# Optimization experiments

Measured on AMD Instinct MI355X. Metric: run time of the kernel, lower is better.

Reference implementation:

```python
import jax, jax.numpy as jnp
import numpy as np

N_HEADS = 2

def setup_inputs() -> dict:
    key = jax.random.key(0)
    ks = jax.random.split(key, 10)
    d, bank, b, t = 192, 1000, 16, 4096
    s = 1.0 / np.sqrt(d)
    return {
        "z": jax.random.normal(ks[0], (b, d, t), jnp.float32),
        "memory_bank": jax.random.normal(ks[1], (d, bank), jnp.float32),
        "Wq": jax.random.normal(ks[2], (d, d), jnp.float32) * s,
        "bq": jax.random.normal(ks[3], (d,), jnp.float32) * 0.02,
        "Wk": jax.random.normal(ks[4], (d, d), jnp.float32) * s,
        "bk": jax.random.normal(ks[5], (d,), jnp.float32) * 0.02,
        "Wv": jax.random.normal(ks[6], (d, d), jnp.float32) * s,
        "bv": jax.random.normal(ks[7], (d,), jnp.float32) * 0.02,
        "Wo": jax.random.normal(ks[8], (d, d), jnp.float32) * s,
        "bo": jax.random.normal(ks[9], (d,), jnp.float32) * 0.02,
    }


def _split_heads(x):
    # x: [b, d, t] -> [b, h, t, dk]  (matches view(b, h, dk, t).transpose(2, 3))
    b, d, t = x.shape
    dk = d // N_HEADS
    return x.reshape(b, N_HEADS, dk, t).transpose(0, 1, 3, 2)


def reference(z, memory_bank, Wq, bq, Wk, bk, Wv, bv, Wo, bo):
    b, d, t = z.shape
    dk = d // N_HEADS
    # memory bank expanded over batch: [b, d, bank]
    c = jnp.broadcast_to(memory_bank[None], (b,) + memory_bank.shape)
    # 1x1 conv projections == per-channel linear
    q = jnp.einsum('oc,bct->bot', Wq, z) + bq[None, :, None]
    k = jnp.einsum('oc,bcs->bos', Wk, c) + bk[None, :, None]
    v = jnp.einsum('oc,bcs->bos', Wv, c) + bv[None, :, None]
    qh = _split_heads(q)  # [b, h, t, dk]
    kh = _split_heads(k)  # [b, h, bank, dk]
    vh = _split_heads(v)  # [b, h, bank, dk]
    scores = jnp.einsum('bhtd,bhsd->bhts', qh, kh) / jnp.sqrt(jnp.asarray(dk, z.dtype))
    p = jax.nn.softmax(scores, axis=-1)  # [b, h, t, bank]
    out = jnp.einsum('bhts,bhsd->bhtd', p, vh)  # [b, h, t, dk]
    out = out.transpose(0, 1, 3, 2).reshape(b, d, t)  # merge heads -> [b, d, t]
    return jnp.einsum('oc,bct->bot', Wo, out) + bo[None, :, None]
```

## Files before the change

### kernel.cpp

```cpp
#include <hip/hip_runtime.h>


typedef float  f32x4  __attribute__((ext_vector_type(4)));
typedef __bf16 bf16;
typedef __bf16 bf16x8 __attribute__((ext_vector_type(8)));

#define B_   16
#define D_   192
#define T_   4096
#define BANK 1000
#define SP   1024
#define DK   96
#define SCALE 0.10206207261596577f
#define LOG2E 1.4426950408889634f

__global__ __launch_bounds__(256) void kv_kernel(
    const float* __restrict__ mb, const float* __restrict__ Wk, const float* __restrict__ bk,
    const float* __restrict__ Wv, const float* __restrict__ bv,
    bf16* __restrict__ ktg, bf16* __restrict__ vtg) {
  int s = blockIdx.x * 256 + threadIdx.x;
  int o = blockIdx.y;
  int h = o / DK, i = o % DK;
  float ak = 0.f, av = 0.f;
  if (s < BANK) {
    ak = bk[o]; av = bv[o];
    for (int c = 0; c < D_; ++c) {
      float m = mb[c * BANK + s];
      ak += Wk[o * D_ + c] * m;
      av += Wv[o * D_ + c] * m;
    }
  }
  ktg[(size_t)(h * SP + s) * DK + i] = (bf16)ak;
  vtg[(size_t)(h * DK + i) * SP + s] = (bf16)av;
}

__global__ __launch_bounds__(256) void zt_kernel(const float* __restrict__ z,
                                                 bf16* __restrict__ zT) {
  __shared__ __align__(16) bf16 sT[64 * 200];
  const int tid = threadIdx.x;
  const int t0 = blockIdx.x * 64, b = blockIdx.y;
#pragma unroll
  for (int it = 0; it < 48; ++it) {
    int e = tid + 256 * it;
    int c = e >> 6, tl = e & 63;
    sT[tl * 200 + c] = (bf16)z[((size_t)b * D_ + c) * T_ + t0 + tl];
  }
  __syncthreads();
#pragma unroll
  for (int it = 0; it < 6; ++it) {
    int g = tid + 256 * it;
    int tl = g / 24, c8 = (g % 24) * 8;
    bf16x8 v = *(const bf16x8*)&sT[tl * 200 + c8];
    *(bf16x8*)&zT[((size_t)b * T_ + t0 + tl) * D_ + c8] = v;
  }
}

template <typename OT>
__global__ __launch_bounds__(256) void proj_kernel(
    const bf16* __restrict__ XT, const float* __restrict__ W,
    const float* __restrict__ bias, OT* __restrict__ Y, float outscale) {
  __shared__ __align__(16) char smem[40960];
  bf16* sA = (bf16*)smem;
  bf16* sB = (bf16*)(smem + 16384);
  float* sE = (float*)smem;

  const int tid = threadIdx.x;
  const int t0 = blockIdx.x * 256, o0 = blockIdx.y * 64, b = blockIdx.z;
  const int lane = tid & 63, wv = tid >> 6;
  const int quad = lane >> 4, l15 = lane & 15;

#pragma unroll
  for (int r = 0; r < 6; ++r) {
    int g = tid + 256 * r;
    int kb = g >> 8, nt = (g >> 6) & 3, qd = (g >> 4) & 3, l5 = g & 15;
    const float* wp = &W[(o0 + nt * 16 + l5) * D_ + kb * 32 + qd * 8];
    f32x4 wa = *(const f32x4*)wp, wb = *(const f32x4*)(wp + 4);
    bf16x8 pk;
#pragma unroll
    for (int u = 0; u < 4; ++u) { pk[u] = (bf16)wa[u]; pk[4 + u] = (bf16)wb[u]; }
    *(bf16x8*)&sB[(size_t)g * 8] = pk;
  }

  f32x4 acc[4][4];
#pragma unroll
  for (int m = 0; m < 4; ++m)
#pragma unroll
    for (int n = 0; n < 4; ++n) acc[m][n] = (f32x4){0.f, 0.f, 0.f, 0.f};

  for (int kb = 0; kb < 6; ++kb) {
    __syncthreads();
#pragma unroll
    for (int r = 0; r < 4; ++r) {
      int g = tid + 256 * r;
      int tg = g >> 6, qd = (g >> 4) & 3, l5 = g & 15;
      bf16x8 v = *(const bf16x8*)&XT[((size_t)b * T_ + t0 + tg * 16 + l5) * D_ +
                                     kb * 32 + qd * 8];
      *(bf16x8*)&sA[(size_t)g * 8] = v;
    }
    __syncthreads();
    bf16x8 bf[4];
#pragma unroll
    for (int n = 0; n < 4; ++n)
      bf[n] = *(const bf16x8*)&sB[(size_t)((kb * 4 + n) * 64 + lane) * 8];
#pragma unroll
    for (int m = 0; m < 4; ++m) {
      bf16x8 af = *(const bf16x8*)&sA[(size_t)((wv * 4 + m) * 64 + lane) * 8];
#pragma unroll
      for (int n = 0; n < 4; ++n)
        acc[m][n] = __builtin_amdgcn_mfma_f32_16x16x32_bf16(af, bf[n], acc[m][n], 0, 0, 0);
    }
  }
  __syncthreads();

  float bs[4];
#pragma unroll
  for (int n = 0; n < 4; ++n) bs[n] = bias[o0 + n * 16 + l15];
  float* se = sE + wv * 1088;
#pragma unroll
  for (int m = 0; m < 4; ++m) {
#pragma unroll
    for (int n = 0; n < 4; ++n)
#pragma unroll
      for (int r = 0; r < 4; ++r)
        se[(quad * 4 + r) * 68 + n * 16 + l15] = (acc[m][n][r] + bs[n]) * outscale;
#pragma unroll
    for (int oo = 0; oo < 16; ++oo) {
      int ol = oo * 4 + quad;
      Y[((size_t)b * D_ + o0 + ol) * T_ + t0 + wv * 64 + m * 16 + l15] =
          (OT)se[l15 * 68 + ol];
    }
  }
}

__global__ __launch_bounds__(512) void attn_kernel(
    const bf16* __restrict__ qws, const bf16* __restrict__ ktg,
    const bf16* __restrict__ vtg, bf16* __restrict__ owsT) {
  __shared__ __align__(16) char smem[32768];
  bf16* kt = (bf16*)smem;
  bf16* vt = (bf16*)(smem + 12288);
  bf16* sP = (bf16*)(smem + 24576);
  bf16* qt = (bf16*)smem;

  const int tid = threadIdx.x;
  const int t0 = blockIdx.x * 128, h = blockIdx.y, b = blockIdx.z;
  const int lane = tid & 63, wv = tid >> 6;
  const int quad = lane >> 4, l15 = lane & 15;

  const bf16* kb_g = ktg + (size_t)h * SP * DK;
  const bf16* vb_g = vtg + (size_t)h * DK * SP;

  const bf16* sp_ptr[3];
  int sp_str[3];
#pragma unroll
  for (int r = 0; r < 3; ++r) {
    int g = tid + 512 * r;
    if (g < 768) {
      int kb = g >> 8, n = (g >> 6) & 3, qd = (g >> 4) & 3, l5 = g & 15;
      sp_ptr[r] = kb_g + (size_t)(n * 16 + l5) * DK + kb * 32 + qd * 8;
      sp_str[r] = 64 * DK;
    } else {
      int gv = g - 768, blk = gv >> 6;
      int kbv = blk / 6, n = blk % 6, qd = (gv >> 4) & 3, l5 = gv & 15;
      sp_ptr[r] = vb_g + (size_t)(n * 16 + l5) * SP + kbv * 32 + qd * 8;
      sp_str[r] = 64;
    }
  }
  bf16x8 kreg[3];
#pragma unroll
  for (int r = 0; r < 3; ++r) kreg[r] = *(const bf16x8*)sp_ptr[r];

#pragma unroll
  for (int r = 0; r < 3; ++r) {
    int g8 = tid + 512 * r;
    int i = g8 >> 4, t8 = (g8 & 15) * 8;
    bf16x8 v = *(const bf16x8*)&qws[((size_t)(b * D_ + h * DK + i)) * T_ + t0 + t8];
    int kb = i >> 5, qd = (i >> 3) & 3, j = i & 7;
#pragma unroll
    for (int tt = 0; tt < 8; ++tt) {
      int t = t8 + tt;
      qt[(size_t)((kb * 8 + (t >> 4)) * 64 + qd * 16 + (t & 15)) * 8 + j] = v[tt];
    }
  }
  __syncthreads();
  bf16x8 qf[3];
#pragma unroll
  for (int kb = 0; kb < 3; ++kb)
    qf[kb] = *(const bf16x8*)&qt[(size_t)((kb * 8 + wv) * 64 + lane) * 8];

  f32x4 oacc[6];
#pragma unroll
  for (int n = 0; n < 6; ++n) oacc[n] = (f32x4){0.f, 0.f, 0.f, 0.f};
  float m_run[4] = {-1e30f, -1e30f, -1e30f, -1e30f};
  float l_run[4] = {0.f, 0.f, 0.f, 0.f};

  for (int ch = 0; ch < 16; ++ch) {
    __syncthreads();
#pragma unroll
    for (int r = 0; r < 3; ++r)
      *(bf16x8*)(smem + (size_t)(tid + 512 * r) * 16) = kreg[r];
    __syncthreads();
    if (ch < 15) {
#pragma unroll
      for (int r = 0; r < 3; ++r) {
        sp_ptr[r] += sp_str[r];
        kreg[r] = *(const bf16x8*)sp_ptr[r];
      }
    }

    f32x4 sacc[4];
#pragma unroll
    for (int n = 0; n < 4; ++n) sacc[n] = (f32x4){0.f, 0.f, 0.f, 0.f};
#pragma unroll
    for (int kb = 0; kb < 3; ++kb) {
#pragma unroll
      for (int n = 0; n < 4; ++n) {
        bf16x8 bfm = *(const bf16x8*)&kt[(size_t)((kb * 4 + n) * 64 + lane) * 8];
        sacc[n] = __builtin_amdgcn_mfma_f32_16x16x32_bf16(qf[kb], bfm, sacc[n], 0, 0, 0);
      }
    }
    if (ch == 15) {
#pragma unroll
      for (int r = 0; r < 4; ++r) {
        if (l15 >= 8) sacc[2][r] = -1e30f;
        sacc[3][r] = -1e30f;
      }
    }

    float mc[4];
#pragma unroll
    for (int r = 0; r < 4; ++r) {
      float m0 = fmaxf(fmaxf(sacc[0][r], sacc[1][r]), fmaxf(sacc[2][r], sacc[3][r]));
      m0 = fmaxf(m0, __shfl_xor(m0, 1, 64));
      m0 = fmaxf(m0, __shfl_xor(m0, 2, 64));
      m0 = fmaxf(m0, __shfl_xor(m0, 4, 64));
      m0 = fmaxf(m0, __shfl_xor(m0, 8, 64));
      mc[r] = m0;
    }
    bool keep = (mc[0] - m_run[0] <= 8.f) && (mc[1] - m_run[1] <= 8.f) &&
                (mc[2] - m_run[2] <= 8.f) && (mc[3] - m_run[3] <= 8.f);
    if (!__all(keep)) {
#pragma unroll
      for (int r = 0; r < 4; ++r) {
        float mn = fmaxf(m_run[r], mc[r]);
        float al = exp2f(m_run[r] - mn);
        m_run[r] = mn;
        l_run[r] *= al;
#pragma unroll
        for (int n = 0; n < 6; ++n) oacc[n][r] *= al;
      }
    }
    float pr[4][4];
#pragma unroll
    for (int r = 0; r < 4; ++r) {
      float ls = 0.f;
#pragma unroll
      for (int n = 0; n < 4; ++n) { pr[n][r] = exp2f(sacc[n][r] - m_run[r]); ls += pr[n][r]; }
      ls += __shfl_xor(ls, 1, 64);
      ls += __shfl_xor(ls, 2, 64);
      ls += __shfl_xor(ls, 4, 64);
      ls += __shfl_xor(ls, 8, 64);
      l_run[r] += ls;
    }

#pragma unroll
    for (int kb = 0; kb < 2; ++kb) {
#pragma unroll
      for (int nn = 0; nn < 2; ++nn) {
        int n = kb * 2 + nn;
        int qd2 = (nn << 1) | (l15 >> 3), j = l15 & 7;
#pragma unroll
        for (int r = 0; r < 4; ++r)
          sP[(size_t)(wv * 64 + qd2 * 16 + quad * 4 + (r ^ quad)) * 8 + j] =
              (bf16)pr[n][r];
      }
      bf16x8 pa = *(const bf16x8*)&sP[(size_t)(wv * 64 + (lane ^ ((lane >> 2) & 3))) * 8];
#pragma unroll
      for (int n2 = 0; n2 < 6; ++n2) {
        bf16x8 vf = *(const bf16x8*)&vt[(size_t)((kb * 6 + n2) * 64 + lane) * 8];
        oacc[n2] = __builtin_amdgcn_mfma_f32_16x16x32_bf16(pa, vf, oacc[n2], 0, 0, 0);
      }
    }
  }

  float inv[4];
#pragma unroll
  for (int r = 0; r < 4; ++r) inv[r] = 1.0f / l_run[r];
  __syncthreads();
  bf16* sOw = (bf16*)smem + wv * (96 * 17);
#pragma unroll
  for (int n2 = 0; n2 < 6; ++n2)
#pragma unroll
    for (int r = 0; r < 4; ++r)
      sOw[(n2 * 16 + l15) * 17 + quad * 4 + r] = (bf16)(oacc[n2][r] * inv[r]);
#pragma unroll
  for (int r2 = 0; r2 < 24; ++r2) {
    int g = r2 * 64 + lane;
    int tl = g / 96, i = g % 96;
    owsT[((size_t)b * T_ + t0 + wv * 16 + tl) * D_ + h * DK + i] = sOw[i * 17 + tl];
  }
}

extern "C" void kernel_launch(void* const* d_in, const int* in_sizes, int n_in,
                              void* d_out, int out_size, void* d_ws, size_t ws_size,
                              hipStream_t stream) {
  const float* z  = (const float*)d_in[0];
  const float* mb = (const float*)d_in[1];
  const float* Wq = (const float*)d_in[2];
  const float* bq = (const float*)d_in[3];
  const float* Wk = (const float*)d_in[4];
  const float* bk = (const float*)d_in[5];
  const float* Wv = (const float*)d_in[6];
  const float* bv = (const float*)d_in[7];
  const float* Wo = (const float*)d_in[8];
  const float* bo = (const float*)d_in[9];
  float* out = (float*)d_out;

  bf16* ktg  = (bf16*)d_ws;
  bf16* vtg  = ktg + 2 * SP * DK;
  bf16* zT   = vtg + 2 * DK * SP;
  bf16* owsT = zT + (size_t)B_ * T_ * D_;
  bf16* qws  = owsT + (size_t)B_ * T_ * D_;

  kv_kernel        <<<dim3(SP / 256, D_),    256, 0, stream>>>(mb, Wk, bk, Wv, bv, ktg, vtg);
  zt_kernel        <<<dim3(T_ / 64, B_),     256, 0, stream>>>(z, zT);
  proj_kernel<bf16><<<dim3(T_ / 256, 3, B_), 256, 0, stream>>>(zT, Wq, bq, qws, SCALE * LOG2E);
  attn_kernel      <<<dim3(T_ / 128, 2, B_), 512, 0, stream>>>(qws, ktg, vtg, owsT);
  proj_kernel<float><<<dim3(T_ / 256, 3, B_), 256, 0, stream>>>(owsT, Wo, bo, out, 1.0f);
}
```

Measured before the change: 300.0 us.

## Merge KV and transpose launches, prefetch proj operands, swizzle attention LDS

Merges the K/V projection kernel and the z transpose kernel into a single launch, with blocks picking their role from blockIdx.y. This removes one kernel launch and lets the two independent jobs run at the same time. The projection GEMM now loads the next k-block of activations into registers before the MFMAs run, overlapping global loads with compute. The attention kernel's Q and P shared-memory layouts gain XOR swizzles meant to cut LDS bank conflicts, at the cost of extra index arithmetic and register pressure.

```diff
diff --git a/kernel.cpp b/kernel.cpp
--- a/kernel.cpp
+++ b/kernel.cpp
@@ -14,44 +14,46 @@
 #define SCALE 0.10206207261596577f
 #define LOG2E 1.4426950408889634f
 
-__global__ __launch_bounds__(256) void kv_kernel(
-    const float* __restrict__ mb, const float* __restrict__ Wk, const float* __restrict__ bk,
+__global__ __launch_bounds__(256) void pre_kernel(
+    const float* __restrict__ z, bf16* __restrict__ zT,
+    const float* __restrict__ mb,
+    const float* __restrict__ Wk, const float* __restrict__ bk,
     const float* __restrict__ Wv, const float* __restrict__ bv,
     bf16* __restrict__ ktg, bf16* __restrict__ vtg) {
-  int s = blockIdx.x * 256 + threadIdx.x;
-  int o = blockIdx.y;
-  int h = o / DK, i = o % DK;
-  float ak = 0.f, av = 0.f;
-  if (s < BANK) {
-    ak = bk[o]; av = bv[o];
-    for (int c = 0; c < D_; ++c) {
-      float m = mb[c * BANK + s];
-      ak += Wk[o * D_ + c] * m;
-      av += Wv[o * D_ + c] * m;
-    }
-  }
-  ktg[(size_t)(h * SP + s) * DK + i] = (bf16)ak;
-  vtg[(size_t)(h * DK + i) * SP + s] = (bf16)av;
-}
-
-__global__ __launch_bounds__(256) void zt_kernel(const float* __restrict__ z,
-                                                 bf16* __restrict__ zT) {
   __shared__ __align__(16) bf16 sT[64 * 200];
   const int tid = threadIdx.x;
-  const int t0 = blockIdx.x * 64, b = blockIdx.y;
-#pragma unroll
-  for (int it = 0; it < 48; ++it) {
-    int e = tid + 256 * it;
-    int c = e >> 6, tl = e & 63;
-    sT[tl * 200 + c] = (bf16)z[((size_t)b * D_ + c) * T_ + t0 + tl];
-  }
-  __syncthreads();
-#pragma unroll
-  for (int it = 0; it < 6; ++it) {
-    int g = tid + 256 * it;
-    int tl = g / 24, c8 = (g % 24) * 8;
-    bf16x8 v = *(const bf16x8*)&sT[tl * 200 + c8];
-    *(bf16x8*)&zT[((size_t)b * T_ + t0 + tl) * D_ + c8] = v;
+  if (blockIdx.y < 16) {
+    const int t0 = blockIdx.x * 64, b = blockIdx.y;
+#pragma unroll
+    for (int it = 0; it < 48; ++it) {
+      int e = tid + 256 * it;
+      int c = e >> 6, tl = e & 63;
+      sT[tl * 200 + c] = (bf16)z[((size_t)b * D_ + c) * T_ + t0 + tl];
+    }
+    __syncthreads();
+#pragma unroll
+    for (int it = 0; it < 6; ++it) {
+      int g = tid + 256 * it;
+      int tl = g / 24, c8 = (g % 24) * 8;
+      bf16x8 v = *(const bf16x8*)&sT[tl * 200 + c8];
+      *(bf16x8*)&zT[((size_t)b * T_ + t0 + tl) * D_ + c8] = v;
+    }
+  } else {
+    int idx = (blockIdx.y - 16) * 64 + blockIdx.x;
+    int s = (idx & 3) * 256 + tid;
+    int o = idx >> 2;
+    int h = o / DK, i = o % DK;
+    float ak = 0.f, av = 0.f;
+    if (s < BANK) {
+      ak = bk[o]; av = bv[o];
+      for (int c = 0; c < D_; ++c) {
+        float m = mb[c * BANK + s];
+        ak += Wk[o * D_ + c] * m;
+        av += Wv[o * D_ + c] * m;
+      }
+    }
+    ktg[(size_t)(h * SP + s) * DK + i] = (bf16)ak;
+    vtg[(size_t)(h * DK + i) * SP + s] = (bf16)av;
   }
 }
 
@@ -69,6 +71,17 @@
   const int lane = tid & 63, wv = tid >> 6;
   const int quad = lane >> 4, l15 = lane & 15;
 
+  const bf16* ap[4];
+#pragma unroll
+  for (int r = 0; r < 4; ++r) {
+    int g = tid + 256 * r;
+    int tg = g >> 6, qd = (g >> 4) & 3, l5 = g & 15;
+    ap[r] = &XT[((size_t)b * T_ + t0 + tg * 16 + l5) * D_ + qd * 8];
+  }
+  bf16x8 areg[4];
+#pragma unroll
+  for (int r = 0; r < 4; ++r) areg[r] = *(const bf16x8*)ap[r];
+
 #pragma unroll
   for (int r = 0; r < 6; ++r) {
     int g = tid + 256 * r;
@@ -90,14 +103,14 @@
   for (int kb = 0; kb < 6; ++kb) {
     __syncthreads();
 #pragma unroll
-    for (int r = 0; r < 4; ++r) {
-      int g = tid + 256 * r;
-      int tg = g >> 6, qd = (g >> 4) & 3, l5 = g & 15;
-      bf16x8 v = *(const bf16x8*)&XT[((size_t)b * T_ + t0 + tg * 16 + l5) * D_ +
-                                     kb * 32 + qd * 8];
-      *(bf16x8*)&sA[(size_t)g * 8] = v;
-    }
-    __syncthreads();
+    for (int r = 0; r < 4; ++r)
+      *(bf16x8*)&sA[(size_t)(tid + 256 * r) * 8] = areg[r];
+    __syncthreads();
+    if (kb < 5) {
+#pragma unroll
+      for (int r = 0; r < 4; ++r)
+        areg[r] = *(const bf16x8*)(ap[r] + (kb + 1) * 32);
+    }
     bf16x8 bf[4];
 #pragma unroll
     for (int n = 0; n < 4; ++n)
@@ -178,14 +191,19 @@
 #pragma unroll
     for (int tt = 0; tt < 8; ++tt) {
       int t = t8 + tt;
-      qt[(size_t)((kb * 8 + (t >> 4)) * 64 + qd * 16 + (t & 15)) * 8 + j] = v[tt];
+      int G = (kb * 8 + (t >> 4)) * 64 + qd * 16 + (t & 15);
+      int Gs = G ^ ((G >> 6) & 7);
+      qt[(size_t)Gs * 8 + j] = v[tt];
     }
   }
   __syncthreads();
   bf16x8 qf[3];
 #pragma unroll
-  for (int kb = 0; kb < 3; ++kb)
-    qf[kb] = *(const bf16x8*)&qt[(size_t)((kb * 8 + wv) * 64 + lane) * 8];
+  for (int kb = 0; kb < 3; ++kb) {
+    int G = (kb * 8 + wv) * 64 + lane;
+    int Gs = G ^ ((G >> 6) & 7);
+    qf[kb] = *(const bf16x8*)&qt[(size_t)Gs * 8];
+  }
 
   f32x4 oacc[6];
 #pragma unroll
@@ -269,11 +287,14 @@
         int n = kb * 2 + nn;
         int qd2 = (nn << 1) | (l15 >> 3), j = l15 & 7;
 #pragma unroll
-        for (int r = 0; r < 4; ++r)
-          sP[(size_t)(wv * 64 + qd2 * 16 + quad * 4 + (r ^ quad)) * 8 + j] =
-              (bf16)pr[n][r];
-      }
-      bf16x8 pa = *(const bf16x8*)&sP[(size_t)(wv * 64 + (lane ^ ((lane >> 2) & 3))) * 8];
+        for (int r = 0; r < 4; ++r) {
+          int g0 = qd2 * 16 + quad * 4 + r;
+          int gs = g0 ^ ((g0 >> 3) & 7);
+          sP[(size_t)(wv * 64 + gs) * 8 + j] = (bf16)pr[n][r];
+        }
+      }
+      int gl = lane ^ ((lane >> 3) & 7);
+      bf16x8 pa = *(const bf16x8*)&sP[(size_t)(wv * 64 + gl) * 8];
 #pragma unroll
       for (int n2 = 0; n2 < 6; ++n2) {
         bf16x8 vf = *(const bf16x8*)&vt[(size_t)((kb * 6 + n2) * 64 + lane) * 8];
@@ -321,9 +342,10 @@
   bf16* owsT = zT + (size_t)B_ * T_ * D_;
   bf16* qws  = owsT + (size_t)B_ * T_ * D_;
 
-  kv_kernel        <<<dim3(SP / 256, D_),    256, 0, stream>>>(mb, Wk, bk, Wv, bv, ktg, vtg);
-  zt_kernel        <<<dim3(T_ / 64, B_),     256, 0, stream>>>(z, zT);
-  proj_kernel<bf16><<<dim3(T_ / 256, 3, B_), 256, 0, stream>>>(zT, Wq, bq, qws, SCALE * LOG2E);
-  attn_kernel      <<<dim3(T_ / 128, 2, B_), 512, 0, stream>>>(qws, ktg, vtg, owsT);
+  pre_kernel        <<<dim3(64, 28),          256, 0, stream>>>(z, zT, mb, Wk, bk, Wv, bv,
+                                                                ktg, vtg);
+  proj_kernel<bf16> <<<dim3(T_ / 256, 3, B_), 256, 0, stream>>>(zT, Wq, bq, qws,
+                                                                SCALE * LOG2E);
+  attn_kernel       <<<dim3(T_ / 128, 2, B_), 512, 0, stream>>>(qws, ktg, vtg, owsT);
   proj_kernel<float><<<dim3(T_ / 256, 3, B_), 256, 0, stream>>>(owsT, Wo, bo, out, 1.0f);
 }
```

Measured after the change: 282.8 us. -5.7%, faster.
